# Kernel optimization log

Measured on AMD Instinct MI355X. Metric: run time of the kernel, lower is better.

Reference implementation:

```python
import jax, jax.numpy as jnp
import numpy as np

# --- static config (mirrors init_kwargs) ---
B, N, CBEV = 4, 4, 64
D, FH, FW = 41, 16, 44          # depth bins, feature H/W after downsample
OGH, OGW, DS = 256, 704, 16     # original image dims, downsample
NX, NY, NZ = 240, 240, 1        # BEV grid (x, y, z)
DX = np.array([0.4, 0.4, 20.0], np.float32)            # voxel size
BX = np.array([-47.8, -47.8, 0.0], np.float32)          # voxel grid origin (bound+dx/2)


def _frustum():
    # [D, FH, FW, 3] with (u_pixel, v_pixel, depth); UD discretization 4..44 step 1
    ds = (4.0 + np.arange(D, dtype=np.float32)).reshape(D, 1, 1) * np.ones((1, FH, FW), np.float32)
    xs = np.linspace(0.0, OGW - 1, FW, dtype=np.float32).reshape(1, 1, FW) * np.ones((D, FH, 1), np.float32)
    ys = np.linspace(0.0, OGH - 1, FH, dtype=np.float32).reshape(1, FH, 1) * np.ones((D, 1, FW), np.float32)
    return jnp.asarray(np.stack([xs, ys, ds], axis=-1))


def setup_inputs() -> dict:
    key = jax.random.key(0)
    x = jax.random.normal(key, (B, N, D, FH, FW, CBEV), dtype=jnp.float32)
    # realistic camera rig: 4 cameras at yaw 0/90/180/270 deg, pinhole intrinsics
    intr = np.zeros((N, 3, 3), np.float32)
    rot = np.zeros((N, 3, 3), np.float32)
    tr = np.zeros((N, 3), np.float32)
    cam2ego = np.array([[0, 0, 1], [-1, 0, 0], [0, -1, 0]], np.float32)  # cam z-fwd -> ego x-fwd
    for n in range(N):
        intr[n] = np.array([[500.0, 0.0, OGW / 2.0], [0.0, 500.0, OGH / 2.0], [0.0, 0.0, 1.0]], np.float32)
        yaw = 2.0 * np.pi * n / N
        c, s = np.cos(yaw), np.sin(yaw)
        Rz = np.array([[c, -s, 0], [s, c, 0], [0, 0, 1]], np.float32)
        rot[n] = Rz @ cam2ego
        tr[n] = np.array([1.5 * c, 1.5 * s, 1.6], np.float32)
    rots = jnp.asarray(np.broadcast_to(rot, (B, N, 3, 3)).copy())
    trans = jnp.asarray(np.broadcast_to(tr, (B, N, 3)).copy())
    intrins = jnp.asarray(np.broadcast_to(intr, (B, N, 3, 3)).copy())
    post_rots = jnp.asarray(np.broadcast_to(np.eye(3, dtype=np.float32), (B, N, 3, 3)).copy())
    post_trans = jnp.zeros((B, N, 3), jnp.float32)
    return {"x": x, "rots": rots, "trans": trans, "intrins": intrins,
            "post_rots": post_rots, "post_trans": post_trans}


def reference(x, rots, trans, intrins, post_rots, post_trans):
    # --- get_geometry: frustum pixel/depth points -> ego-frame xyz ---
    frustum = _frustum()                                            # [D,FH,FW,3]
    pts = frustum[None, None] - post_trans[:, :, None, None, None, :]
    pts = jnp.einsum('bnij,bndhwj->bndhwi', jnp.linalg.inv(post_rots), pts)
    pts = jnp.concatenate([pts[..., :2] * pts[..., 2:3], pts[..., 2:3]], axis=-1)
    combine = rots @ jnp.linalg.inv(intrins)
    pts = jnp.einsum('bnij,bndhwj->bndhwi', combine, pts) + trans[:, :, None, None, None, :]
    # --- voxel_pooling: quantize, mask OOB, segment-sum into dense BEV grid ---
    dx = jnp.asarray(DX)
    bx = jnp.asarray(BX)
    vox = ((pts - (bx - dx / 2.0)) / dx).astype(jnp.int32)          # trunc, same as torch .long()
    vx, vy, vz = vox[..., 0], vox[..., 1], vox[..., 2]              # [B,N,D,FH,FW]
    kept = (vx >= 0) & (vx < NX) & (vy >= 0) & (vy < NY) & (vz >= 0) & (vz < NZ)
    bidx = jnp.arange(B, dtype=jnp.int32)[:, None, None, None, None]
    nvox = B * NZ * NY * NX
    lin = bidx * (NZ * NY * NX) + vz * (NY * NX) + vy * NX + vx
    lin = jnp.where(kept, lin, nvox).reshape(-1)                    # invalid -> dummy bin
    feats = x.reshape(-1, CBEV)                                     # [Nprime, C]
    sums = jax.ops.segment_sum(feats, lin, num_segments=nvox + 1)[:nvox]
    final = sums.reshape(B, NZ, NY, NX, CBEV).transpose(0, 1, 4, 2, 3)  # [B,Z,C,Y,X]
    # torch: cat(final.unbind(dim=2), 1) on [B,C,Z,Y,X] -> [B, Z*C, Y, X] z-major
    return final.reshape(B, NZ * CBEV, NY, NX)
```

## Files before the change

### kernel.cpp

```cpp
#include <hip/hip_runtime.h>

#define BB   4
#define NNC  4
#define DDEP 41
#define FHH  16
#define FWW  44
#define CC   64
#define NXX  240
#define NYY  240
#define NVOX (BB*NYY*NXX)
#define NTRI (BB*NNC*DDEP*FWW)

typedef float f4 __attribute__((ext_vector_type(4)));

__device__ __forceinline__ void inv3x3_upper_f32(const float K[9], float o[9]) {
    float a00 = __fdiv_rn(1.0f, K[0]);
    float a11 = __fdiv_rn(1.0f, K[4]);
    float a22 = __fdiv_rn(1.0f, K[8]);
    float b01 = __fmul_rn(-a11, __fmul_rn(a00, K[1]));
    float x0 = __fadd_rn(__fmul_rn(a00, K[2]), __fmul_rn(b01, K[5]));
    float x1 = __fmul_rn(a11, K[5]);
    float b02 = __fmul_rn(-a22, x0);
    float b12 = __fmul_rn(-a22, x1);
    o[0]=a00; o[1]=b01; o[2]=b02;
    o[3]=0.0f; o[4]=a11; o[5]=b12;
    o[6]=0.0f; o[7]=0.0f; o[8]=a22;
}

__global__ void __launch_bounds__(256) splat(
        const float* __restrict__ x,
        const float* __restrict__ rots,
        const float* __restrict__ trans,
        const float* __restrict__ intrins,
        const float* __restrict__ post_rots,
        const float* __restrict__ post_trans,
        float* __restrict__ out) {
    int tid  = threadIdx.x;
    int wid  = tid >> 6;
    int lane = tid & 63;
    int sub  = lane >> 4;
    int h    = lane & 15;
    int tbase = (blockIdx.x*4 + wid)*4;
    int tri  = tbase + sub;

    int w    = tri % FWW;
    int rest = tri / FWW;
    int d    = rest % DDEP;
    int bn   = rest / DDEP;

    float K[9], PR[9], R[9];
    #pragma unroll
    for (int i = 0; i < 9; ++i) {
        K[i]  = intrins[bn*9 + i];
        PR[i] = post_rots[bn*9 + i];
        R[i]  = rots[bn*9 + i];
    }
    float Ki[9], PRi[9];
    inv3x3_upper_f32(K, Ki);
    inv3x3_upper_f32(PR, PRi);
    float C[9];
    #pragma unroll
    for (int i = 0; i < 3; ++i)
        #pragma unroll
        for (int j = 0; j < 3; ++j) {
            float s = __fmul_rn(R[i*3+0], Ki[0*3+j]);
            s = __fadd_rn(s, __fmul_rn(R[i*3+1], Ki[1*3+j]));
            s = __fadd_rn(s, __fmul_rn(R[i*3+2], Ki[2*3+j]));
            C[i*3+j] = s;
        }
    float ptx = post_trans[bn*3+0], pty = post_trans[bn*3+1], ptz = post_trans[bn*3+2];
    float trx = trans[bn*3+0], try_ = trans[bn*3+1], trz = trans[bn*3+2];

    float u  = (float)((double)w * (703.0/43.0));
    float v  = (float)((double)h * 17.0);
    float dd = (float)(4 + d);

    float p0x = __fsub_rn(u,  ptx);
    float p0y = __fsub_rn(v,  pty);
    float p0z = __fsub_rn(dd, ptz);
    float p1x = __fadd_rn(__fadd_rn(__fmul_rn(PRi[0],p0x), __fmul_rn(PRi[1],p0y)), __fmul_rn(PRi[2],p0z));
    float p1y = __fadd_rn(__fadd_rn(__fmul_rn(PRi[3],p0x), __fmul_rn(PRi[4],p0y)), __fmul_rn(PRi[5],p0z));
    float p1z = __fadd_rn(__fadd_rn(__fmul_rn(PRi[6],p0x), __fmul_rn(PRi[7],p0y)), __fmul_rn(PRi[8],p0z));
    float p2x = __fmul_rn(p1x, p1z);
    float p2y = __fmul_rn(p1y, p1z);
    float p2z = p1z;
    float ex = __fadd_rn(__fadd_rn(__fmul_rn(C[0],p2x), __fmul_rn(C[1],p2y)), __fmul_rn(C[2],p2z));
    float ey = __fadd_rn(__fadd_rn(__fmul_rn(C[3],p2x), __fmul_rn(C[4],p2y)), __fmul_rn(C[5],p2z));
    float ez = __fadd_rn(__fadd_rn(__fmul_rn(C[6],p2x), __fmul_rn(C[7],p2y)), __fmul_rn(C[8],p2z));
    float gx = __fadd_rn(ex, trx);
    float gy = __fadd_rn(ey, try_);
    float gz = __fadd_rn(ez, trz);

    float qx = __fdiv_rn(__fsub_rn(gx, -48.0f), 0.4f);
    float qy = __fdiv_rn(__fsub_rn(gy, -48.0f), 0.4f);
    float qz = __fdiv_rn(__fsub_rn(gz, -10.0f), 20.0f);
    int vx = (int)qx;
    int vy = (int)qy;
    int vz = (int)qz;

    bool kept = (vx >= 0) & (vx < NXX) & (vy >= 0) & (vy < NYY) & (vz == 0);
    unsigned long long bal = __ballot(kept);

    int b_ = bn / NNC;
    int vb = b_*(NYY*NXX) + vy*NXX + vx;

    int hq = lane >> 4, c4 = lane & 15;
    #pragma unroll
    for (int s = 0; s < 4; ++s) {
        unsigned int m = (unsigned int)((bal >> (s*16)) & 0xFFFFull);
        if (m == 0u) continue;

        int vbs = __shfl(vb, s*16);
        int tris = tbase + s;
        int ws    = tris % FWW;
        int rests = tris / FWW;
        int ds    = rests % DDEP;
        int bns   = rests / DDEP;
        const float* xb = x + (size_t)((bns*DDEP + ds)*FHH*FWW + ws)*CC + c4*4;

        f4 acc = (f4)(0.0f);
        #pragma unroll
        for (int r = 0; r < 4; ++r) {
            int hh = r*4 + hq;
            if ((m >> hh) & 1u) {
                f4 t = *(const f4*)(xb + (size_t)hh*(FWW*CC));
                acc += t;
            }
        }
        acc.x += __shfl_xor(acc.x, 16); acc.y += __shfl_xor(acc.y, 16);
        acc.z += __shfl_xor(acc.z, 16); acc.w += __shfl_xor(acc.w, 16);
        acc.x += __shfl_xor(acc.x, 32); acc.y += __shfl_xor(acc.y, 32);
        acc.z += __shfl_xor(acc.z, 32); acc.w += __shfl_xor(acc.w, 32);

        if (lane < 16) {
            int bb = vbs / (NYY*NXX);
            int yx = vbs - bb*(NYY*NXX);
            float* ob = out + (size_t)bb*(CC*NYY*NXX) + yx;
            atomicAdd(&ob[(size_t)(c4*4 + 0)*(NYY*NXX)], acc.x);
            atomicAdd(&ob[(size_t)(c4*4 + 1)*(NYY*NXX)], acc.y);
            atomicAdd(&ob[(size_t)(c4*4 + 2)*(NYY*NXX)], acc.z);
            atomicAdd(&ob[(size_t)(c4*4 + 3)*(NYY*NXX)], acc.w);
        }
    }
}

extern "C" void kernel_launch(void* const* d_in, const int* in_sizes, int n_in,
                              void* d_out, int out_size, void* d_ws, size_t ws_size,
                              hipStream_t stream) {
    const float* x          = (const float*)d_in[0];
    const float* rots       = (const float*)d_in[1];
    const float* trans      = (const float*)d_in[2];
    const float* intrins    = (const float*)d_in[3];
    const float* post_rots  = (const float*)d_in[4];
    const float* post_trans = (const float*)d_in[5];
    float* out = (float*)d_out;

    hipMemsetAsync(out, 0, (size_t)out_size, stream);
    splat<<<NTRI/16, 256, 0, stream>>>(x, rots, trans, intrins, post_rots,
                                       post_trans, out);
}
```

Measured before the change: 269.5 us.

## Replace global atomic splat with per-cell-block gather scan into shared memory

Splits the kernel into a geometry pass that writes one packed record (voxel index plus h-mask) per ray triple to workspace, and an assemble pass where each block owns 128 BEV cells, scans every record, gathers the matching features into an LDS accumulator and writes the output once with nontemporal stores. This drops the output memset and the strided global atomics. In exchange, each of the 1800 blocks rescans all ~29k records, which adds redundant read traffic and ballot work that could dominate.

```diff
diff --git a/kernel.cpp b/kernel.cpp
--- a/kernel.cpp
+++ b/kernel.cpp
@@ -10,6 +10,10 @@
 #define NYY  240
 #define NVOX (BB*NYY*NXX)
 #define NTRI (BB*NNC*DDEP*FWW)
+#define CELLS 128
+#define NBLK (NVOX/CELLS)
+
+#define W_REC 0
 
 typedef float f4 __attribute__((ext_vector_type(4)));
 
@@ -27,21 +31,19 @@
     o[6]=0.0f; o[7]=0.0f; o[8]=a22;
 }
 
-__global__ void __launch_bounds__(256) splat(
-        const float* __restrict__ x,
+__global__ void __launch_bounds__(256) geom_rec(
         const float* __restrict__ rots,
         const float* __restrict__ trans,
         const float* __restrict__ intrins,
         const float* __restrict__ post_rots,
         const float* __restrict__ post_trans,
-        float* __restrict__ out) {
+        unsigned long long* __restrict__ rec) {
     int tid  = threadIdx.x;
     int wid  = tid >> 6;
     int lane = tid & 63;
     int sub  = lane >> 4;
     int h    = lane & 15;
-    int tbase = (blockIdx.x*4 + wid)*4;
-    int tri  = tbase + sub;
+    int tri  = (blockIdx.x*4 + wid)*4 + sub;
 
     int w    = tri % FWW;
     int rest = tri / FWW;
@@ -100,47 +102,98 @@
 
     bool kept = (vx >= 0) & (vx < NXX) & (vy >= 0) & (vy < NYY) & (vz == 0);
     unsigned long long bal = __ballot(kept);
-
-    int b_ = bn / NNC;
-    int vb = b_*(NYY*NXX) + vy*NXX + vx;
+    unsigned int mask = (unsigned int)((bal >> (sub*16)) & 0xFFFFull);
+
+    if (h == 0) {
+        int b_ = bn / NNC;
+        int vb = b_*(NYY*NXX) + vy*NXX + vx;
+        unsigned long long r = mask ? (((unsigned long long)mask << 32)
+                                      | (unsigned int)vb)
+                                    : 0ull;
+        rec[tri] = r;
+    }
+}
+
+__global__ void __launch_bounds__(256) assemble_scan(
+        const float* __restrict__ x,
+        const unsigned long long* __restrict__ rec,
+        float* __restrict__ out) {
+    __shared__ float acc[CELLS*65];
+    int tid  = threadIdx.x;
+    int lane = tid & 63;
+    int v0   = blockIdx.x * CELLS;
+
+    for (int i = tid; i < CELLS*65; i += 256) acc[i] = 0.0f;
+    __syncthreads();
 
     int hq = lane >> 4, c4 = lane & 15;
-    #pragma unroll
-    for (int s = 0; s < 4; ++s) {
-        unsigned int m = (unsigned int)((bal >> (s*16)) & 0xFFFFull);
-        if (m == 0u) continue;
-
-        int vbs = __shfl(vb, s*16);
-        int tris = tbase + s;
-        int ws    = tris % FWW;
-        int rests = tris / FWW;
-        int ds    = rests % DDEP;
-        int bns   = rests / DDEP;
-        const float* xb = x + (size_t)((bns*DDEP + ds)*FHH*FWW + ws)*CC + c4*4;
-
-        f4 acc = (f4)(0.0f);
+
+    for (int k0 = 0; k0 < 113; k0 += 4) {
+        unsigned long long r[4];
         #pragma unroll
-        for (int r = 0; r < 4; ++r) {
-            int hh = r*4 + hq;
-            if ((m >> hh) & 1u) {
-                f4 t = *(const f4*)(xb + (size_t)hh*(FWW*CC));
-                acc += t;
+        for (int u2 = 0; u2 < 4; ++u2) {
+            int idx = (k0 + u2)*256 + tid;
+            r[u2] = (idx < NTRI) ? rec[idx] : 0ull;
+        }
+        #pragma unroll
+        for (int u2 = 0; u2 < 4; ++u2) {
+            unsigned int vb = (unsigned int)r[u2];
+            unsigned int m_ = (unsigned int)(r[u2] >> 32);
+            bool match = (m_ != 0u) && ((unsigned int)(vb - (unsigned int)v0) < (unsigned int)CELLS);
+            unsigned long long mm = __ballot(match);
+            while (mm) {
+                int j = __ffsll(mm) - 1;
+                mm &= mm - 1;
+                unsigned int vbj = (unsigned int)__shfl((int)vb, j);
+                unsigned int mj  = (unsigned int)__shfl((int)m_, j);
+                int trij = (k0 + u2)*256 + (tid & ~63) + j;
+
+                int w    = trij % FWW;
+                int rest = trij / FWW;
+                int d    = rest % DDEP;
+                int bn   = rest / DDEP;
+                const float* xb = x + (size_t)((bn*DDEP + d)*FHH*FWW + w)*CC + c4*4;
+
+                f4 a = (f4)(0.0f);
+                #pragma unroll
+                for (int rr = 0; rr < 4; ++rr) {
+                    int hh = rr*4 + hq;
+                    if ((mj >> hh) & 1u) {
+                        f4 t = *(const f4*)(xb + (size_t)hh*(FWW*CC));
+                        a += t;
+                    }
+                }
+                a.x += __shfl_xor(a.x, 16); a.y += __shfl_xor(a.y, 16);
+                a.z += __shfl_xor(a.z, 16); a.w += __shfl_xor(a.w, 16);
+                a.x += __shfl_xor(a.x, 32); a.y += __shfl_xor(a.y, 32);
+                a.z += __shfl_xor(a.z, 32); a.w += __shfl_xor(a.w, 32);
+
+                if (lane < 16) {
+                    float* ap = &acc[(vbj - (unsigned int)v0)*65 + c4*4];
+                    atomicAdd(ap + 0, a.x);
+                    atomicAdd(ap + 1, a.y);
+                    atomicAdd(ap + 2, a.z);
+                    atomicAdd(ap + 3, a.w);
+                }
             }
         }
-        acc.x += __shfl_xor(acc.x, 16); acc.y += __shfl_xor(acc.y, 16);
-        acc.z += __shfl_xor(acc.z, 16); acc.w += __shfl_xor(acc.w, 16);
-        acc.x += __shfl_xor(acc.x, 32); acc.y += __shfl_xor(acc.y, 32);
-        acc.z += __shfl_xor(acc.z, 32); acc.w += __shfl_xor(acc.w, 32);
-
-        if (lane < 16) {
-            int bb = vbs / (NYY*NXX);
-            int yx = vbs - bb*(NYY*NXX);
-            float* ob = out + (size_t)bb*(CC*NYY*NXX) + yx;
-            atomicAdd(&ob[(size_t)(c4*4 + 0)*(NYY*NXX)], acc.x);
-            atomicAdd(&ob[(size_t)(c4*4 + 1)*(NYY*NXX)], acc.y);
-            atomicAdd(&ob[(size_t)(c4*4 + 2)*(NYY*NXX)], acc.z);
-            atomicAdd(&ob[(size_t)(c4*4 + 3)*(NYY*NXX)], acc.w);
-        }
+    }
+    __syncthreads();
+
+    int b   = v0 / (NYY*NXX);
+    int yx0 = v0 - b*(NYY*NXX);
+    float* outb = out + (size_t)b*(CC*NYY*NXX) + yx0;
+    #pragma unroll
+    for (int it = 0; it < 8; ++it) {
+        int s  = it*256 + tid;
+        int c  = s >> 5;
+        int xi = s & 31;
+        f4 f;
+        f.x = acc[(xi*4 + 0)*65 + c];
+        f.y = acc[(xi*4 + 1)*65 + c];
+        f.z = acc[(xi*4 + 2)*65 + c];
+        f.w = acc[(xi*4 + 3)*65 + c];
+        __builtin_nontemporal_store(f, (f4*)(outb + (size_t)c*(NYY*NXX) + xi*4));
     }
 }
 
@@ -155,7 +208,9 @@
     const float* post_trans = (const float*)d_in[5];
     float* out = (float*)d_out;
 
-    hipMemsetAsync(out, 0, (size_t)out_size, stream);
-    splat<<<NTRI/16, 256, 0, stream>>>(x, rots, trans, intrins, post_rots,
-                                       post_trans, out);
-}
+    unsigned long long* rec = (unsigned long long*)((char*)d_ws + W_REC);
+
+    geom_rec<<<NTRI/16, 256, 0, stream>>>(rots, trans, intrins, post_rots,
+                                          post_trans, rec);
+    assemble_scan<<<NBLK, 256, 0, stream>>>(x, rec, out);
+}
```

After: 329.8 us. 22.4% more time.
